# Kernel tuning notes

Hardware: AMD Instinct MI355X
Metric: run time of the kernel (lower is better)

## Reference

```python
import jax, jax.numpy as jnp
import numpy as np


def setup_inputs() -> dict:
    key = jax.random.key(0)
    k1, k2 = jax.random.split(key)
    inp = jax.random.normal(k1, (32, 1, 128, 128), dtype=jnp.float32)
    mask = (jax.random.uniform(k2, (32, 1, 1, 128)) < 0.25).astype(jnp.float32)
    return {"input": inp, "mask": mask}


def reference(input, mask):
    # Faithful to KSpaceMap.forward: `mask` is accepted but never used there.
    # Original: k = RFFT(x) (unnormalized full 2D FFT via torch.rfft onesided=False),
    # repeat W times, zero all but column i, then IFFT2 (torch.ifft, includes 1/(H*W)),
    # keep the real channel -> out[b, i, h, w].
    # Because the mask is a one-hot frequency column, ifft2 factorizes analytically:
    #   ifft2(onehot_col_i(k)) = (1/W) * ifft_h(k)[:, i] outer exp(2*pi*j*i*w/W)
    # which avoids materializing the [B, W, 2, H, W] repeated k-space.
    B, _, H, W = input.shape
    x = input[:, 0, :, :]                              # [B, H, W]
    k = jnp.fft.fft2(x)                                # [B, H, W] complex, unnormalized FFT
    A = jnp.fft.ifft(k, axis=-2)                       # ifft over height (1/H included): [B, H, W]
    w = jnp.arange(W)
    phase = 2.0 * jnp.pi * jnp.outer(w, w).astype(jnp.float32) / W   # [W(i), W(w)]
    Pr = jnp.cos(phase) / W                            # real part of DFT basis / W
    Pi = jnp.sin(phase) / W                            # imag part of DFT basis / W
    # out[b, i, h, w] = Re(A[b, h, i] * P[i, w])
    out = (jnp.einsum('bhi,iw->bihw', A.real.astype(jnp.float32), Pr)
           - jnp.einsum('bhi,iw->bihw', A.imag.astype(jnp.float32), Pi))
    return out
```

## Files before the change

### kernel.cpp

```cpp
#include <hip/hip_runtime.h>
#include <math.h>


#define IPG 8

__global__ __launch_bounds__(256, 2) void kspace_fused(const float* __restrict__ x,
                                                       float* __restrict__ out) {
    const int blk = blockIdx.x;
    const int b   = blk >> 4;
    const int ig  = blk & 15;
    const int t   = threadIdx.x;

    __shared__ float xl[128 * 129];
    __shared__ __align__(16) float ct[128], st[128];
    __shared__ __align__(16) float ar_[128], ai_[128];
    __shared__ __align__(16) float cw[128], sw[128];

    if (t < 128) {
        float s, c;
        sincospif((float)t * (1.0f / 64.0f), &s, &c);
        ct[t] = c;
        st[t] = s;
    }

    const float* xb = x + (size_t)b * 16384;
#pragma unroll
    for (int r = 0; r < 64; ++r) {
        const int idx = t + r * 256;
        const int h   = idx >> 7;
        const int u   = idx & 127;
        xl[h * 129 + u] = xb[idx];
    }
    __syncthreads();

    const int h    = t >> 1;
    const int half = t & 1;
    const float* xrow = &xl[h * 129 + half * 64];

    for (int ii = 0; ii < IPG; ++ii) {
        const int i = ig * IPG + ii;

        float ar = 0.0f, aiv = 0.0f;
        const int ustart = half * 64;
#pragma unroll
        for (int j = 0; j < 64; ++j) {
            const int k = (i * (ustart + j)) & 127;
            const float xv = xrow[j];
            ar  = fmaf(xv,  ct[k], ar);
            aiv = fmaf(xv, -st[k], aiv);
        }
        ar  += __shfl_xor(ar, 1);
        aiv += __shfl_xor(aiv, 1);
        if (half == 0) {
            ar_[h] = ar  * (1.0f / 128.0f);
            ai_[h] = aiv * (1.0f / 128.0f);
        }
        if (t < 128) {
            const int k2 = (i * t) & 127;
            cw[t] = ct[k2];
            sw[t] = st[k2];
        }
        __syncthreads();

        float4* __restrict__ o4 = (float4*)(out + ((size_t)(b * 128 + i)) * 16384);
        const float4* cw4 = (const float4*)cw;
        const float4* sw4 = (const float4*)sw;
#pragma unroll
        for (int j = 0; j < 16; ++j) {
            const int q  = t + j * 256;
            const int hh = q >> 5;
            const int w4 = q & 31;
            const float a  = ar_[hh];
            const float bb = ai_[hh];
            const float4 cc = cw4[w4];
            const float4 ss = sw4[w4];
            float4 v;
            v.x = a * cc.x - bb * ss.x;
            v.y = a * cc.y - bb * ss.y;
            v.z = a * cc.z - bb * ss.z;
            v.w = a * cc.w - bb * ss.w;
            o4[q] = v;
        }
        __syncthreads();
    }
}

extern "C" void kernel_launch(void* const* d_in, const int* in_sizes, int n_in,
                              void* d_out, int out_size, void* d_ws, size_t ws_size,
                              hipStream_t stream) {
    const float* x = (const float*)d_in[0];
    float* out = (float*)d_out;
    kspace_fused<<<dim3(512), dim3(256), 0, stream>>>(x, out);
}
```

Measured before the change: 50.15 us.

## Exploit conjugate symmetry of output columns and drop shared memory staging

For real input, out[b,128-i] equals out[b,i], so each block computes columns i and 128-i together and writes the result twice. That halves the DFT arithmetic. Input rows are now held in registers instead of LDS, twiddles come from a rotation recurrence seeded by sincospif, and coefficients are passed between lanes with shuffles instead of shared memory plus barriers. Stores use nontemporal hints. The kernel is likely bound by its write traffic, so the extra compute saving may matter little, and the recurrence adds a small rounding error.

```diff
diff --git a/kernel.cpp b/kernel.cpp
--- a/kernel.cpp
+++ b/kernel.cpp
@@ -2,86 +2,90 @@
 #include <math.h>
 
 
-#define IPG 8
+typedef float f32x4 __attribute__((ext_vector_type(4)));
 
-__global__ __launch_bounds__(256, 2) void kspace_fused(const float* __restrict__ x,
-                                                       float* __restrict__ out) {
-    const int blk = blockIdx.x;
-    const int b   = blk >> 4;
-    const int ig  = blk & 15;
-    const int t   = threadIdx.x;
+__global__ __launch_bounds__(256) void kspace_v3(const float* __restrict__ x,
+                                                 float* __restrict__ out) {
+    const int blk  = blockIdx.x;
+    const int b    = blk / 33;
+    const int g    = blk % 33;
+    const int t    = threadIdx.x;
+    const int wv   = t >> 6;
+    const int lane = t & 63;
+    const int hh0  = lane >> 1;
+    const int h    = wv * 32 + hh0;
+    const int half = lane & 1;
 
-    __shared__ float xl[128 * 129];
-    __shared__ __align__(16) float ct[128], st[128];
-    __shared__ __align__(16) float ar_[128], ai_[128];
-    __shared__ __align__(16) float cw[128], sw[128];
-
-    if (t < 128) {
-        float s, c;
-        sincospif((float)t * (1.0f / 64.0f), &s, &c);
-        ct[t] = c;
-        st[t] = s;
+    const float* xp = x + ((size_t)b * 128 + h) * 128 + half * 64;
+    float xs[64];
+#pragma unroll
+    for (int j = 0; j < 16; ++j) {
+        const f32x4 v = ((const f32x4*)xp)[j];
+        xs[4 * j + 0] = v.x;
+        xs[4 * j + 1] = v.y;
+        xs[4 * j + 2] = v.z;
+        xs[4 * j + 3] = v.w;
     }
 
-    const float* xb = x + (size_t)b * 16384;
-#pragma unroll
-    for (int r = 0; r < 64; ++r) {
-        const int idx = t + r * 256;
-        const int h   = idx >> 7;
-        const int u   = idx & 127;
-        xl[h * 129 + u] = xb[idx];
-    }
-    __syncthreads();
+    const int nb = (g < 32) ? 2 : 1;
+#pragma unroll 1
+    for (int ib = 0; ib < nb; ++ib) {
+        const int i = (g < 32) ? (g * 2 + ib) : 64;
 
-    const int h    = t >> 1;
-    const int half = t & 1;
-    const float* xrow = &xl[h * 129 + half * 64];
-
-    for (int ii = 0; ii < IPG; ++ii) {
-        const int i = ig * IPG + ii;
+        float sstep, cstep;
+        sincospif((float)i * (1.0f / 64.0f), &sstep, &cstep);
+        const float dc = cstep, ds = -sstep;
 
         float ar = 0.0f, aiv = 0.0f;
-        const int ustart = half * 64;
 #pragma unroll
-        for (int j = 0; j < 64; ++j) {
-            const int k = (i * (ustart + j)) & 127;
-            const float xv = xrow[j];
-            ar  = fmaf(xv,  ct[k], ar);
-            aiv = fmaf(xv, -st[k], aiv);
+        for (int ch = 0; ch < 2; ++ch) {
+            const int u0 = half * 64 + ch * 32;
+            const int a0 = (i * u0) & 127;
+            float s0, c0;
+            sincospif((float)a0 * (1.0f / 64.0f), &s0, &c0);
+            float cr = c0, ci = -s0;
+#pragma unroll
+            for (int j2 = 0; j2 < 32; ++j2) {
+                const float xv = xs[ch * 32 + j2];
+                ar  = fmaf(xv, cr, ar);
+                aiv = fmaf(xv, ci, aiv);
+                const float ncr = fmaf(cr, dc, -ci * ds);
+                ci = fmaf(cr, ds, ci * dc);
+                cr = ncr;
+            }
         }
         ar  += __shfl_xor(ar, 1);
         aiv += __shfl_xor(aiv, 1);
-        if (half == 0) {
-            ar_[h] = ar  * (1.0f / 128.0f);
-            ai_[h] = aiv * (1.0f / 128.0f);
+        ar  *= (1.0f / 128.0f);
+        aiv *= (1.0f / 128.0f);
+
+        const int wbase = (lane & 31) * 4;
+        float cwv[4], swv[4];
+#pragma unroll
+        for (int c = 0; c < 4; ++c) {
+            const int k = (i * (wbase + c)) & 127;
+            sincospif((float)k * (1.0f / 64.0f), &swv[c], &cwv[c]);
         }
-        if (t < 128) {
-            const int k2 = (i * t) & 127;
-            cw[t] = ct[k2];
-            sw[t] = st[k2];
-        }
-        __syncthreads();
 
-        float4* __restrict__ o4 = (float4*)(out + ((size_t)(b * 128 + i)) * 16384);
-        const float4* cw4 = (const float4*)cw;
-        const float4* sw4 = (const float4*)sw;
+        f32x4* const o1 = (f32x4*)out + (size_t)(b * 128 + i) * 4096;
+        f32x4* const o2 = (f32x4*)out + (size_t)(b * 128 + (128 - i)) * 4096;
+        const bool dup = (i >= 1 && i <= 63);
+
 #pragma unroll
         for (int j = 0; j < 16; ++j) {
-            const int q  = t + j * 256;
-            const int hh = q >> 5;
-            const int w4 = q & 31;
-            const float a  = ar_[hh];
-            const float bb = ai_[hh];
-            const float4 cc = cw4[w4];
-            const float4 ss = sw4[w4];
-            float4 v;
-            v.x = a * cc.x - bb * ss.x;
-            v.y = a * cc.y - bb * ss.y;
-            v.z = a * cc.z - bb * ss.z;
-            v.w = a * cc.w - bb * ss.w;
-            o4[q] = v;
+            const int hhl = (lane >> 5) + 2 * j;
+            const int src = 2 * hhl;
+            const float a  = __shfl(ar,  src);
+            const float bb = __shfl(aiv, src);
+            f32x4 v;
+            v.x = fmaf(a, cwv[0], -bb * swv[0]);
+            v.y = fmaf(a, cwv[1], -bb * swv[1]);
+            v.z = fmaf(a, cwv[2], -bb * swv[2]);
+            v.w = fmaf(a, cwv[3], -bb * swv[3]);
+            const int idx = (wv * 32 + hhl) * 32 + (lane & 31);
+            __builtin_nontemporal_store(v, &o1[idx]);
+            if (dup) __builtin_nontemporal_store(v, &o2[idx]);
         }
-        __syncthreads();
     }
 }
 
@@ -90,5 +94,5 @@
                               hipStream_t stream) {
     const float* x = (const float*)d_in[0];
     float* out = (float*)d_out;
-    kspace_fused<<<dim3(512), dim3(256), 0, stream>>>(x, out);
+    kspace_v3<<<dim3(1056), dim3(256), 0, stream>>>(x, out);
 }
```

Result: slower. 59.51 us (+18.7%).
